# Performance work log

Hardware: AMD Instinct MI355X
Metric: run time of the kernel (lower is better)

Reference implementation:

```python
import jax, jax.numpy as jnp
import numpy as np

N_NODES = 100000
N_EDGES = 1600000
IN_CH, HID_CH, OUT_CH = 128, 128, 64


def _spmm(row, col, val, x, n):
    # COO sparse @ dense: out[r] += val_e * x[col_e]
    gathered = val[:, None] * x[col]  # [E, d]
    return jax.ops.segment_sum(gathered, row, num_segments=n)


def setup_inputs() -> dict:
    key = jax.random.key(0)
    ks = jax.random.split(key, 8)
    x = jax.random.normal(ks[0], (N_NODES, IN_CH), dtype=jnp.float32)
    adj_row = jax.random.randint(ks[1], (N_EDGES,), 0, N_NODES)
    adj_col = jax.random.randint(ks[2], (N_EDGES,), 0, N_NODES)
    adj_val = jax.random.uniform(ks[3], (N_EDGES,), dtype=jnp.float32)
    w1 = jax.random.normal(ks[4], (IN_CH, HID_CH), dtype=jnp.float32) * (1.0 / np.sqrt(IN_CH))
    b1 = jax.random.normal(ks[5], (HID_CH,), dtype=jnp.float32) * 0.01
    w2 = jax.random.normal(ks[6], (HID_CH, OUT_CH), dtype=jnp.float32) * (1.0 / np.sqrt(HID_CH))
    b2 = jax.random.normal(ks[7], (OUT_CH,), dtype=jnp.float32) * 0.01
    return {"x": x, "adj_row": adj_row, "adj_col": adj_col, "adj_val": adj_val,
            "w1": w1, "b1": b1, "w2": w2, "b2": b2}


def reference(x, adj_row, adj_col, adj_val, w1, b1, w2, b2):
    n = x.shape[0]
    # layer 1: spmm -> linear -> relu
    h = _spmm(adj_row, adj_col, adj_val, x, n)
    h = jax.nn.relu(h @ w1 + b1)
    # layer 2: spmm -> linear
    h = _spmm(adj_row, adj_col, adj_val, h, n)
    return h @ w2 + b2
```

## Files before the change

### kernel.cpp

```cpp
#include <hip/hip_runtime.h>


typedef __bf16 v8bf __attribute__((ext_vector_type(8)));
typedef float  v4f  __attribute__((ext_vector_type(4)));
typedef unsigned v2u __attribute__((ext_vector_type(2)));

#define AS1 __attribute__((address_space(1)))
#define AS3 __attribute__((address_space(3)))

#define MAXB 800

__device__ __forceinline__ unsigned short f2bf(float f) {
    unsigned u = __float_as_uint(f);
    unsigned r = u + 0x7fffu + ((u >> 16) & 1u);
    return (unsigned short)(r >> 16);
}

__device__ __forceinline__ unsigned ldsaddr(const void* p) {
    return (unsigned)(unsigned long long)(const AS3 char*)p;
}

__device__ __forceinline__ v2u tr16(unsigned a) {
    v2u d;
    asm volatile("ds_read_b64_tr_b16 %0, %1" : "=v"(d) : "v"(a));
    return d;
}

__global__ __launch_bounds__(256) void hist_prep(const int* __restrict__ arow,
                                                 int* __restrict__ counts, int E, int B,
                                                 const float* __restrict__ w1,
                                                 const float* __restrict__ w2,
                                                 unsigned short* __restrict__ w1T,
                                                 unsigned short* __restrict__ w2T,
                                                 int* __restrict__ rowptr,
                                                 int2* __restrict__ epkS, int N) {
    const int tid = threadIdx.x;
    int gi = blockIdx.x * 256 + tid;
    if (gi < 16384) {
        int n = gi >> 7, k = gi & 127;
        w1T[gi] = f2bf(w1[k * 128 + n]);
    } else if (gi < 24576) {
        int i2 = gi - 16384;
        int n = i2 >> 7, k = i2 & 127;
        w2T[i2] = f2bf(w2[k * 64 + n]);
    } else if (gi < 24576 + 32) {
        epkS[E + (gi - 24576)] = make_int2(0, 0);
    } else if (gi == 24576 + 32) {
        rowptr[N] = E;
    }
    __shared__ int lh[MAXB];
    for (int i = tid; i < B; i += 256) lh[i] = 0;
    __syncthreads();
    const int base = blockIdx.x * 4096;
#pragma unroll
    for (int j = 0; j < 16; ++j) {
        int i = base + j * 256 + tid;
        if (i < E) atomicAdd(&lh[arow[i] >> 7], 1);
    }
    __syncthreads();
    for (int i = tid; i < B; i += 256) {
        int c = lh[i];
        if (c) atomicAdd(&counts[i], c);
    }
}

__global__ __launch_bounds__(256) void scan_s(const int* __restrict__ counts,
                                              int* __restrict__ boff,
                                              int* __restrict__ gcursor, int B, int E) {
    __shared__ int lds[256];
    const int t = threadIdx.x;
    const int b0 = t * 4;
    int v[4];
    int s = 0;
#pragma unroll
    for (int j = 0; j < 4; ++j) {
        v[j] = (b0 + j < B) ? counts[b0 + j] : 0;
        s += v[j];
    }
    lds[t] = s;
    __syncthreads();
    for (int off = 1; off < 256; off <<= 1) {
        int tmp = 0;
        if (t >= off) tmp = lds[t - off];
        __syncthreads();
        if (t >= off) lds[t] += tmp;
        __syncthreads();
    }
    int run = (t > 0) ? lds[t - 1] : 0;
#pragma unroll
    for (int j = 0; j < 4; ++j) {
        if (b0 + j < B) {
            boff[b0 + j] = run;
            gcursor[b0 + j] = run;
        }
        run += v[j];
    }
    if (t == 255) boff[B] = E;
}

__global__ __launch_bounds__(256) void partition_k(const int* __restrict__ arow,
                                                   const int* __restrict__ acol,
                                                   const float* __restrict__ aval,
                                                   int* __restrict__ gcursor,
                                                   int2* __restrict__ epk, int E, int B) {
    __shared__ int2 ldata[4096];
    __shared__ int ldest[4096];
    __shared__ int lhist[MAXB];
    __shared__ int lscan[MAXB];
    __shared__ int ldelta[MAXB];
    __shared__ int lcur[MAXB];
    __shared__ int stmp[256];
    const int tid = threadIdx.x;
    const int base = blockIdx.x * 4096;
    const int cnt = min(4096, E - base);

    for (int i = tid; i < MAXB; i += 256) {
        lhist[i] = 0;
        lcur[i] = 0;
    }
    __syncthreads();

    int rr[16];
#pragma unroll
    for (int j = 0; j < 16; ++j) {
        int i = base + j * 256 + tid;
        rr[j] = (i < E) ? arow[i] : -1;
        if (rr[j] >= 0) atomicAdd(&lhist[rr[j] >> 7], 1);
    }
    __syncthreads();

    const int b0 = tid * 4;
    int v[4];
    int s = 0;
#pragma unroll
    for (int j = 0; j < 4; ++j) {
        v[j] = (b0 + j < MAXB) ? lhist[b0 + j] : 0;
        s += v[j];
    }
    stmp[tid] = s;
    __syncthreads();
    for (int off = 1; off < 256; off <<= 1) {
        int tmp = 0;
        if (tid >= off) tmp = stmp[tid - off];
        __syncthreads();
        if (tid >= off) stmp[tid] += tmp;
        __syncthreads();
    }
    int run = (tid > 0) ? stmp[tid - 1] : 0;
#pragma unroll
    for (int j = 0; j < 4; ++j) {
        if (b0 + j < MAXB) lscan[b0 + j] = run;
        run += v[j];
    }
    __syncthreads();

    for (int b = tid; b < B; b += 256) {
        int c = lhist[b];
        if (c) ldelta[b] = atomicAdd(&gcursor[b], c) - lscan[b];
    }
    __syncthreads();

#pragma unroll
    for (int j = 0; j < 16; ++j) {
        int i = base + j * 256 + tid;
        if (i < E) {
            int r = rr[j];
            int b = r >> 7;
            int lp = atomicAdd(&lcur[b], 1);
            int slot = lscan[b] + lp;
            int pk = acol[i] | ((r & 127) << 17);
            ldata[slot] = make_int2(pk, __float_as_int(aval[i]));
            ldest[slot] = ldelta[b] + slot;
        }
    }
    __syncthreads();

    for (int s2 = tid; s2 < cnt; s2 += 256) epk[ldest[s2]] = ldata[s2];
}

template <int NC, bool AF32>
__device__ __forceinline__ void gemm_body(const void* __restrict__ A,
                                          const unsigned short* __restrict__ wT,
                                          unsigned short* __restrict__ y, int M,
                                          int bid, char* smem) {
    constexpr int KP = 136;
    constexpr int NT = NC / 16;
    unsigned short* wl = (unsigned short*)smem;
    const int tid = threadIdx.x;
    for (int idx = tid; idx < NC * 16; idx += 256) {
        int n = idx >> 4, kc = idx & 15;
        *(uint4*)&wl[n * KP + kc * 8] = *(const uint4*)&wT[n * 128 + kc * 8];
    }
    __syncthreads();

    const int wave = tid >> 6;
    const int lane = tid & 63;
    const int m = lane & 15;
    const int q = lane >> 4;
    const int rowbase = bid * 64 + wave * 16;
    const int rowc = min(rowbase + m, M - 1);

    v4f acc[NT] = {};
    union LU { uint4 qv; v8bf b; };

#pragma unroll
    for (int ks = 0; ks < 4; ++ks) {
        const int k0 = ks * 32 + q * 8;
        v8bf a;
        if (AF32) {
            const float* Ap = (const float*)A + (size_t)rowc * 128 + k0;
            float4 f0 = *(const float4*)Ap;
            float4 f1 = *(const float4*)(Ap + 4);
            union { unsigned short s[8]; v8bf b; } cv;
            cv.s[0] = f2bf(f0.x); cv.s[1] = f2bf(f0.y);
            cv.s[2] = f2bf(f0.z); cv.s[3] = f2bf(f0.w);
            cv.s[4] = f2bf(f1.x); cv.s[5] = f2bf(f1.y);
            cv.s[6] = f2bf(f1.z); cv.s[7] = f2bf(f1.w);
            a = cv.b;
        } else {
            LU lu;
            lu.qv = *(const uint4*)((const unsigned short*)A + (size_t)rowc * 128 + k0);
            a = lu.b;
        }
#pragma unroll
        for (int nt = 0; nt < NT; ++nt) {
            v8bf b = *(const v8bf*)&wl[(nt * 16 + m) * KP + k0];
            acc[nt] = __builtin_amdgcn_mfma_f32_16x16x32_bf16(a, b, acc[nt], 0, 0, 0);
        }
    }
#pragma unroll
    for (int nt = 0; nt < NT; ++nt) {
#pragma unroll
        for (int r = 0; r < 4; ++r) {
            int orow = rowbase + q * 4 + r;
            if (orow < M) y[(size_t)orow * NC + nt * 16 + m] = f2bf(acc[nt][r]);
        }
    }
}

__global__ __launch_bounds__(256) void sort_gemm1(const int* __restrict__ boff,
                                                  const int2* __restrict__ epk,
                                                  int2* __restrict__ epkS,
                                                  int* __restrict__ rowptr, int N, int B,
                                                  const float* __restrict__ x,
                                                  const unsigned short* __restrict__ w1T,
                                                  unsigned short* __restrict__ y1b) {
    __shared__ __align__(16) char smem[34816];
    const int tid = threadIdx.x;
    if (blockIdx.x >= B) {
        gemm_body<128, true>(x, w1T, y1b, N, blockIdx.x - B, smem);
        return;
    }
    int2* sorted = (int2*)smem;
    int*  sc     = (int*)(smem + 32768);
    int*  lcur   = (int*)(smem + 32768 + 512);
    const int b = blockIdx.x;
    const int s = boff[b], e = boff[b + 1];
    const int cnt = min(e - s, 4096);
    if (tid < 128) sc[tid] = 0;
    __syncthreads();
    for (int i = s + tid; i < e; i += 256) {
        int rl = (epk[i].x >> 17) & 127;
        atomicAdd(&sc[rl], 1);
    }
    __syncthreads();
    int hv = (tid < 128) ? sc[tid] : 0;
    for (int off = 1; off < 128; off <<= 1) {
        int add = 0;
        if (tid < 128 && tid >= off) add = sc[tid - off];
        __syncthreads();
        if (tid < 128 && tid >= off) sc[tid] += add;
        __syncthreads();
    }
    if (tid < 128) {
        int ex = sc[tid] - hv;
        lcur[tid] = ex;
        int r = b * 128 + tid;
        if (r < N) rowptr[r] = s + ex;
    }
    __syncthreads();
    for (int i = s + tid; i < e; i += 256) {
        int2 p = epk[i];
        int rl = (p.x >> 17) & 127;
        int slot = atomicAdd(&lcur[rl], 1);
        if (slot < 4096) sorted[slot] = p;
    }
    __syncthreads();
    for (int i = tid; i < cnt; i += 256) epkS[s + i] = sorted[i];
}

__global__ __launch_bounds__(256) void spmm_gemm2(const int* __restrict__ rowptr,
                                                  const int2* __restrict__ ep,
                                                  const unsigned short* __restrict__ y1b,
                                                  const float* __restrict__ b1,
                                                  const unsigned short* __restrict__ w2T,
                                                  unsigned short* __restrict__ y2b, int N) {
    constexpr int KP = 136;
    __shared__ __align__(1024) char smem[40960];
    const int tid = threadIdx.x;
    const int wave = tid >> 6, lane = tid & 63;
    char* NTc = smem + wave * 10240;
    char* AT0 = NTc + 8192;
    char* AT1 = NTc + 9216;
    const int rowbase = blockIdx.x * 64;
    const int r0 = rowbase + wave * 16;
    const int si = __builtin_amdgcn_readfirstlane(rowptr[min(r0, N)]);
    const int ei = __builtin_amdgcn_readfirstlane(rowptr[min(r0 + 16, N)]);
    const int m = lane & 15, q = lane >> 4;

    float b1v[8];
#pragma unroll
    for (int h = 0; h < 8; ++h) b1v[h] = b1[h * 16 + m];

    const unsigned trB = ldsaddr(NTc) + (unsigned)(q * 256 + m * 8);

    v4f acc[8] = {};

    for (int cb = si; cb < ei; cb += 32) {
        const int2 pe = ep[cb + (lane & 31)];
        const int colg = __shfl(pe.x & 0x1FFFF, lane >> 1);
        const char* gp = (const char*)y1b + ((size_t)(unsigned)colg << 8) + ((lane & 1) << 4);
#pragma unroll
        for (int t = 0; t < 8; ++t)
            __builtin_amdgcn_global_load_lds((const AS1 unsigned*)(gp + t * 32),
                                             (AS3 unsigned*)(NTc + t * 1024),
                                             16, 0, 0);
        const uint4 z4 = make_uint4(0u, 0u, 0u, 0u);
        *(uint4*)(AT0 + lane * 16) = z4;
        *(uint4*)(AT1 + lane * 16) = z4;
        if (lane < 32 && cb + lane < ei) {
            const float v = __int_as_float(pe.y);
            const unsigned short vh = f2bf(v);
            const float vhf = __uint_as_float((unsigned)vh << 16);
            const unsigned short vl = f2bf(v - vhf);
            const int rl4 = (pe.x >> 17) & 15;
            *(unsigned short*)(AT0 + rl4 * 64 + lane * 2) = vh;
            *(unsigned short*)(AT1 + rl4 * 64 + lane * 2) = vl;
        }
        asm volatile("s_waitcnt vmcnt(0)" ::: "memory");
        __builtin_amdgcn_sched_barrier(0);
        v2u tr0[8], tr1[8];
#pragma unroll
        for (int h = 0; h < 8; ++h) {
            tr0[h] = tr16(trB + h * 1024);
            tr1[h] = tr16(trB + h * 1024 + 128);
        }
        const v8bf avh = *(const v8bf*)(AT0 + m * 64 + q * 16);
        const v8bf avl = *(const v8bf*)(AT1 + m * 64 + q * 16);
        asm volatile("s_waitcnt lgkmcnt(0)" ::: "memory");
        __builtin_amdgcn_sched_barrier(0);
#pragma unroll
        for (int h = 0; h < 8; ++h) {
            union { unsigned u[4]; v8bf b; } bu;
            bu.u[0] = tr0[h][0]; bu.u[1] = tr0[h][1];
            bu.u[2] = tr1[h][0]; bu.u[3] = tr1[h][1];
            acc[h] = __builtin_amdgcn_mfma_f32_16x16x32_bf16(avh, bu.b, acc[h], 0, 0, 0);
            acc[h] = __builtin_amdgcn_mfma_f32_16x16x32_bf16(avl, bu.b, acc[h], 0, 0, 0);
        }
    }
    __syncthreads();
    unsigned short* h1 = (unsigned short*)smem;
#pragma unroll
    for (int h = 0; h < 8; ++h) {
#pragma unroll
        for (int r = 0; r < 4; ++r) {
            const float f = fmaxf(acc[h][r] + b1v[h], 0.f);
            h1[(wave * 16 + q * 4 + r) * KP + h * 16 + m] = f2bf(f);
        }
    }
    __syncthreads();

    v4f acc2[4] = {};
#pragma unroll
    for (int ks = 0; ks < 4; ++ks) {
        const int k0 = ks * 32 + q * 8;
        v8bf av = *(const v8bf*)&h1[(wave * 16 + m) * KP + k0];
#pragma unroll
        for (int nt = 0; nt < 4; ++nt) {
            v8bf b = *(const v8bf*)&w2T[(nt * 16 + m) * 128 + k0];
            acc2[nt] = __builtin_amdgcn_mfma_f32_16x16x32_bf16(av, b, acc2[nt], 0, 0, 0);
        }
    }
#pragma unroll
    for (int nt = 0; nt < 4; ++nt) {
#pragma unroll
        for (int r = 0; r < 4; ++r) {
            int orow = rowbase + wave * 16 + q * 4 + r;
            if (orow < N) y2b[(size_t)orow * 64 + nt * 16 + m] = f2bf(acc2[nt][r]);
        }
    }
}

__global__ __launch_bounds__(256) void spmm64(const int* __restrict__ rowptr,
                                              const int2* __restrict__ ep,
                                              const unsigned short* __restrict__ yb,
                                              const float* __restrict__ bias,
                                              float* __restrict__ outp, int N) {
    const int row = (blockIdx.x * 256 + threadIdx.x) >> 6;
    const int lane = threadIdx.x & 63;
    if (row >= N) return;
    const int eslot = lane >> 3;
    const int cb = lane & 7;
    const unsigned* y32 = (const unsigned*)yb;
    const int s = __builtin_amdgcn_readfirstlane(rowptr[row]);
    const int e = __builtin_amdgcn_readfirstlane(rowptr[row + 1]);
    float a[8] = {0.f, 0.f, 0.f, 0.f, 0.f, 0.f, 0.f, 0.f};
    int2 cur[2];
#pragma unroll
    for (int k = 0; k < 2; ++k) cur[k] = ep[s + 8 * k + eslot];
    for (int j = s; j < e; j += 16) {
        int2 nxt[2];
#pragma unroll
        for (int k = 0; k < 2; ++k) nxt[k] = ep[j + 16 + 8 * k + eslot];
        uint4 g[2];
        float v[2];
#pragma unroll
        for (int k = 0; k < 2; ++k) {
            v[k] = (j + 8 * k + eslot < e) ? __int_as_float(cur[k].y) : 0.f;
            if (j + 8 * k < e)
                g[k] = *(const uint4*)(y32 + (((unsigned)(cur[k].x & 0x1FFFF)) << 5) + (cb << 2));
            else
                g[k] = make_uint4(0u, 0u, 0u, 0u);
        }
#pragma unroll
        for (int k = 0; k < 2; ++k) {
            a[0] += v[k] * __uint_as_float(g[k].x << 16);
            a[1] += v[k] * __uint_as_float(g[k].x & 0xffff0000u);
            a[2] += v[k] * __uint_as_float(g[k].y << 16);
            a[3] += v[k] * __uint_as_float(g[k].y & 0xffff0000u);
            a[4] += v[k] * __uint_as_float(g[k].z << 16);
            a[5] += v[k] * __uint_as_float(g[k].z & 0xffff0000u);
            a[6] += v[k] * __uint_as_float(g[k].w << 16);
            a[7] += v[k] * __uint_as_float(g[k].w & 0xffff0000u);
        }
#pragma unroll
        for (int k = 0; k < 2; ++k) cur[k] = nxt[k];
    }
#pragma unroll
    for (int t = 0; t < 8; ++t) a[t] += __shfl_xor(a[t], 8);
#pragma unroll
    for (int t = 0; t < 8; ++t) a[t] += __shfl_xor(a[t], 16);
#pragma unroll
    for (int t = 0; t < 8; ++t) a[t] += __shfl_xor(a[t], 32);
    if (lane < 8) {
        const float4 c0 = *(const float4*)&bias[8 * cb];
        const float4 c1 = *(const float4*)&bias[8 * cb + 4];
        float4 o0 = make_float4(a[0] + c0.x, a[1] + c0.y, a[2] + c0.z, a[3] + c0.w);
        float4 o1 = make_float4(a[4] + c1.x, a[5] + c1.y, a[6] + c1.z, a[7] + c1.w);
        float* op = outp + (size_t)row * 64 + 8 * cb;
        *(float4*)op = o0;
        *(float4*)(op + 4) = o1;
    }
}

extern "C" void kernel_launch(void* const* d_in, const int* in_sizes, int n_in,
                              void* d_out, int out_size, void* d_ws, size_t ws_size,
                              hipStream_t stream) {
    const float* x    = (const float*)d_in[0];
    const int*   arow = (const int*)d_in[1];
    const int*   acol = (const int*)d_in[2];
    const float* aval = (const float*)d_in[3];
    const float* w1   = (const float*)d_in[4];
    const float* b1   = (const float*)d_in[5];
    const float* w2   = (const float*)d_in[6];
    const float* b2   = (const float*)d_in[7];
    float*       out  = (float*)d_out;

    const int N = in_sizes[0] / 128;
    const int E = in_sizes[1];
    const int B = (N + 127) >> 7;

    char* p = (char*)d_ws;
    auto alloc = [&](size_t bytes) {
        char* r = p;
        p += (bytes + 255) & ~(size_t)255;
        return r;
    };
    int*            counts  = (int*)alloc((size_t)MAXB * 4);
    int*            boff    = (int*)alloc((size_t)(MAXB + 1) * 4);
    int*            gcursor = (int*)alloc((size_t)MAXB * 4);
    int*            rowptr  = (int*)alloc((size_t)(N + 1) * 4);
    int2*           epkS    = (int2*)alloc((size_t)(E + 32) * 8);
    unsigned short* w1T     = (unsigned short*)alloc(128 * 128 * 2);
    unsigned short* w2T     = (unsigned short*)alloc(64 * 128 * 2);
    unsigned short* y1b     = (unsigned short*)alloc((size_t)N * 128 * 2);
    int2*           epk     = (int2*)alloc((size_t)E * 8);
    unsigned short* y2b     = (unsigned short*)alloc((size_t)N * 64 * 2);

    const int gemm_blocks = (N + 63) / 64;
    const int pb = (E + 4095) / 4096;

    hipMemsetAsync(counts, 0, (size_t)MAXB * 4, stream);
    hist_prep<<<pb, 256, 0, stream>>>(arow, counts, E, B, w1, w2, w1T, w2T,
                                      rowptr, epkS, N);
    scan_s<<<1, 256, 0, stream>>>(counts, boff, gcursor, B, E);
    partition_k<<<pb, 256, 0, stream>>>(arow, acol, aval, gcursor, epk, E, B);
    sort_gemm1<<<B + gemm_blocks, 256, 0, stream>>>(boff, epk, epkS, rowptr, N, B,
                                                    x, w1T, y1b);
    spmm_gemm2<<<gemm_blocks, 256, 0, stream>>>(rowptr, epkS, y1b, b1, w2T, y2b, N);
    const int spmm_blocks = (N + 3) / 4;
    spmm64<<<spmm_blocks, 256, 0, stream>>>(rowptr, epkS, y2b, b2, out, N);
}
```

Measured before the change: 280.9 us.

## Double-buffer SpMM gather DMA and switch second SpMM to MFMA path

```diff
diff --git a/kernel.cpp b/kernel.cpp
--- a/kernel.cpp
+++ b/kernel.cpp
@@ -289,59 +289,70 @@
     for (int i = tid; i < cnt; i += 256) epkS[s + i] = sorted[i];
 }
 
-__global__ __launch_bounds__(256) void spmm_gemm2(const int* __restrict__ rowptr,
-                                                  const int2* __restrict__ ep,
-                                                  const unsigned short* __restrict__ y1b,
-                                                  const float* __restrict__ b1,
-                                                  const unsigned short* __restrict__ w2T,
-                                                  unsigned short* __restrict__ y2b, int N) {
-    constexpr int KP = 136;
-    __shared__ __align__(1024) char smem[40960];
-    const int tid = threadIdx.x;
-    const int wave = tid >> 6, lane = tid & 63;
-    char* NTc = smem + wave * 10240;
-    char* AT0 = NTc + 8192;
-    char* AT1 = NTc + 9216;
-    const int rowbase = blockIdx.x * 64;
-    const int r0 = rowbase + wave * 16;
-    const int si = __builtin_amdgcn_readfirstlane(rowptr[min(r0, N)]);
-    const int ei = __builtin_amdgcn_readfirstlane(rowptr[min(r0 + 16, N)]);
+template <int NT>
+__device__ __forceinline__ void issue_dma(const unsigned short* __restrict__ yb,
+                                          int colg, int lane, char* NB) {
+    const char* gp = (const char*)yb + ((size_t)(unsigned)colg << (NT == 8 ? 8 : 7)) +
+                     ((lane & 1) << 4);
+#pragma unroll
+    for (int t = 0; t < NT; ++t)
+        __builtin_amdgcn_global_load_lds((const AS1 unsigned*)(gp + t * 32),
+                                         (AS3 unsigned*)(NB + t * 1024), 16, 0, 0);
+}
+
+template <int NT>
+__device__ __forceinline__ void spmm_mfma_pipe(int si, int ei, int E,
+                                               const int2* __restrict__ ep,
+                                               const unsigned short* __restrict__ yb,
+                                               char* NB0, char* NB1, char* AT0, char* AT1,
+                                               int lane, v4f* acc) {
     const int m = lane & 15, q = lane >> 4;
-
-    float b1v[8];
-#pragma unroll
-    for (int h = 0; h < 8; ++h) b1v[h] = b1[h * 16 + m];
-
-    const unsigned trB = ldsaddr(NTc) + (unsigned)(q * 256 + m * 8);
-
-    v4f acc[8] = {};
-
-    for (int cb = si; cb < ei; cb += 32) {
-        const int2 pe = ep[cb + (lane & 31)];
-        const int colg = __shfl(pe.x & 0x1FFFF, lane >> 1);
-        const char* gp = (const char*)y1b + ((size_t)(unsigned)colg << 8) + ((lane & 1) << 4);
-#pragma unroll
-        for (int t = 0; t < 8; ++t)
-            __builtin_amdgcn_global_load_lds((const AS1 unsigned*)(gp + t * 32),
-                                             (AS3 unsigned*)(NTc + t * 1024),
-                                             16, 0, 0);
+    const int l31 = lane & 31;
+    const unsigned trBo = (unsigned)(q * 256 + m * 8);
+    const int nch = (ei - si + 31) >> 5;
+    if (nch <= 0) return;
+    int2 peA = ep[min(si + l31, E + 31)];
+    {
+        int colg0 = __shfl(peA.x & 0x1FFFF, lane >> 1);
+        issue_dma<NT>(yb, colg0, lane, NB0);
+    }
+    int2 peB = ep[min(si + 32 + l31, E + 31)];
+#pragma unroll 1
+    for (int c = 0; c < nch; ++c) {
+        char* curN = (c & 1) ? NB1 : NB0;
+        char* nxtN = (c & 1) ? NB0 : NB1;
+        const int cb = si + c * 32;
+        const bool more = (c + 1 < nch);
+        int2 peC = ep[min(cb + 64 + l31, E + 31)];
+        __builtin_amdgcn_sched_barrier(0);
+        if (more) {
+            int colgN = __shfl(peB.x & 0x1FFFF, lane >> 1);
+            issue_dma<NT>(yb, colgN, lane, nxtN);
+        }
+        __builtin_amdgcn_sched_barrier(0);
         const uint4 z4 = make_uint4(0u, 0u, 0u, 0u);
         *(uint4*)(AT0 + lane * 16) = z4;
         *(uint4*)(AT1 + lane * 16) = z4;
-        if (lane < 32 && cb + lane < ei) {
-            const float v = __int_as_float(pe.y);
+        if (lane < 32 && cb + l31 < ei) {
+            const float v = __int_as_float(peA.y);
             const unsigned short vh = f2bf(v);
             const float vhf = __uint_as_float((unsigned)vh << 16);
             const unsigned short vl = f2bf(v - vhf);
-            const int rl4 = (pe.x >> 17) & 15;
-            *(unsigned short*)(AT0 + rl4 * 64 + lane * 2) = vh;
-            *(unsigned short*)(AT1 + rl4 * 64 + lane * 2) = vl;
-        }
-        asm volatile("s_waitcnt vmcnt(0)" ::: "memory");
+            const int rl4 = (peA.x >> 17) & 15;
+            *(unsigned short*)(AT0 + rl4 * 64 + l31 * 2) = vh;
+            *(unsigned short*)(AT1 + rl4 * 64 + l31 * 2) = vl;
+        }
+        if (more) {
+            if constexpr (NT == 8) asm volatile("s_waitcnt vmcnt(9)" ::: "memory");
+            else                   asm volatile("s_waitcnt vmcnt(5)" ::: "memory");
+        } else {
+            asm volatile("s_waitcnt vmcnt(0)" ::: "memory");
+        }
         __builtin_amdgcn_sched_barrier(0);
-        v2u tr0[8], tr1[8];
-#pragma unroll
-        for (int h = 0; h < 8; ++h) {
+        const unsigned trB = ldsaddr(curN) + trBo;
+        v2u tr0[NT], tr1[NT];
+#pragma unroll
+        for (int h = 0; h < NT; ++h) {
             tr0[h] = tr16(trB + h * 1024);
             tr1[h] = tr16(trB + h * 1024 + 128);
         }
@@ -350,21 +361,46 @@
         asm volatile("s_waitcnt lgkmcnt(0)" ::: "memory");
         __builtin_amdgcn_sched_barrier(0);
 #pragma unroll
-        for (int h = 0; h < 8; ++h) {
+        for (int h = 0; h < NT; ++h) {
             union { unsigned u[4]; v8bf b; } bu;
             bu.u[0] = tr0[h][0]; bu.u[1] = tr0[h][1];
             bu.u[2] = tr1[h][0]; bu.u[3] = tr1[h][1];
             acc[h] = __builtin_amdgcn_mfma_f32_16x16x32_bf16(avh, bu.b, acc[h], 0, 0, 0);
             acc[h] = __builtin_amdgcn_mfma_f32_16x16x32_bf16(avl, bu.b, acc[h], 0, 0, 0);
         }
-    }
+        peA = peB;
+        peB = peC;
+    }
+}
+
+__global__ __launch_bounds__(128) void spmm_gemm2(const int* __restrict__ rowptr,
+                                                  const int2* __restrict__ ep,
+                                                  const unsigned short* __restrict__ y1b,
+                                                  const float* __restrict__ b1,
+                                                  const unsigned short* __restrict__ w2T,
+                                                  unsigned short* __restrict__ y2b,
+                                                  int N, int E) {
+    constexpr int KP = 136;
+    __shared__ __align__(1024) char smem[36864];
+    const int tid = threadIdx.x;
+    const int wave = tid >> 6, lane = tid & 63;
+    char* W = smem + wave * 18432;
+    const int rowbase = blockIdx.x * 32;
+    const int r0 = rowbase + wave * 16;
+    const int si = __builtin_amdgcn_readfirstlane(rowptr[min(r0, N)]);
+    const int ei = __builtin_amdgcn_readfirstlane(rowptr[min(r0 + 16, N)]);
+    const int m = lane & 15, q = lane >> 4;
+
+    v4f acc[8] = {};
+    spmm_mfma_pipe<8>(si, ei, E, ep, y1b, W, W + 8192, W + 16384, W + 17408, lane, acc);
     __syncthreads();
     unsigned short* h1 = (unsigned short*)smem;
 #pragma unroll
     for (int h = 0; h < 8; ++h) {
+        const float bv = b1[h * 16 + m];
 #pragma unroll
         for (int r = 0; r < 4; ++r) {
-            const float f = fmaxf(acc[h][r] + b1v[h], 0.f);
+            const float f = fmaxf(acc[h][r] + bv, 0.f);
             h1[(wave * 16 + q * 4 + r) * KP + h * 16 + m] = f2bf(f);
         }
     }
@@ -395,61 +431,27 @@
                                               const int2* __restrict__ ep,
                                               const unsigned short* __restrict__ yb,
                                               const float* __restrict__ bias,
-                                              float* __restrict__ outp, int N) {
-    const int row = (blockIdx.x * 256 + threadIdx.x) >> 6;
-    const int lane = threadIdx.x & 63;
-    if (row >= N) return;
-    const int eslot = lane >> 3;
-    const int cb = lane & 7;
-    const unsigned* y32 = (const unsigned*)yb;
-    const int s = __builtin_amdgcn_readfirstlane(rowptr[row]);
-    const int e = __builtin_amdgcn_readfirstlane(rowptr[row + 1]);
-    float a[8] = {0.f, 0.f, 0.f, 0.f, 0.f, 0.f, 0.f, 0.f};
-    int2 cur[2];
-#pragma unroll
-    for (int k = 0; k < 2; ++k) cur[k] = ep[s + 8 * k + eslot];
-    for (int j = s; j < e; j += 16) {
-        int2 nxt[2];
-#pragma unroll
-        for (int k = 0; k < 2; ++k) nxt[k] = ep[j + 16 + 8 * k + eslot];
-        uint4 g[2];
-        float v[2];
-#pragma unroll
-        for (int k = 0; k < 2; ++k) {
-            v[k] = (j + 8 * k + eslot < e) ? __int_as_float(cur[k].y) : 0.f;
-            if (j + 8 * k < e)
-                g[k] = *(const uint4*)(y32 + (((unsigned)(cur[k].x & 0x1FFFF)) << 5) + (cb << 2));
-            else
-                g[k] = make_uint4(0u, 0u, 0u, 0u);
-        }
-#pragma unroll
-        for (int k = 0; k < 2; ++k) {
-            a[0] += v[k] * __uint_as_float(g[k].x << 16);
-            a[1] += v[k] * __uint_as_float(g[k].x & 0xffff0000u);
-            a[2] += v[k] * __uint_as_float(g[k].y << 16);
-            a[3] += v[k] * __uint_as_float(g[k].y & 0xffff0000u);
-            a[4] += v[k] * __uint_as_float(g[k].z << 16);
-            a[5] += v[k] * __uint_as_float(g[k].z & 0xffff0000u);
-            a[6] += v[k] * __uint_as_float(g[k].w << 16);
-            a[7] += v[k] * __uint_as_float(g[k].w & 0xffff0000u);
-        }
-#pragma unroll
-        for (int k = 0; k < 2; ++k) cur[k] = nxt[k];
-    }
-#pragma unroll
-    for (int t = 0; t < 8; ++t) a[t] += __shfl_xor(a[t], 8);
-#pragma unroll
-    for (int t = 0; t < 8; ++t) a[t] += __shfl_xor(a[t], 16);
-#pragma unroll
-    for (int t = 0; t < 8; ++t) a[t] += __shfl_xor(a[t], 32);
-    if (lane < 8) {
-        const float4 c0 = *(const float4*)&bias[8 * cb];
-        const float4 c1 = *(const float4*)&bias[8 * cb + 4];
-        float4 o0 = make_float4(a[0] + c0.x, a[1] + c0.y, a[2] + c0.z, a[3] + c0.w);
-        float4 o1 = make_float4(a[4] + c1.x, a[5] + c1.y, a[6] + c1.z, a[7] + c1.w);
-        float* op = outp + (size_t)row * 64 + 8 * cb;
-        *(float4*)op = o0;
-        *(float4*)(op + 4) = o1;
+                                              float* __restrict__ outp, int N, int E) {
+    __shared__ __align__(1024) char smem[40960];
+    const int tid = threadIdx.x;
+    const int wave = tid >> 6, lane = tid & 63;
+    char* W = smem + wave * 10240;
+    const int r0 = blockIdx.x * 64 + wave * 16;
+    const int si = __builtin_amdgcn_readfirstlane(rowptr[min(r0, N)]);
+    const int ei = __builtin_amdgcn_readfirstlane(rowptr[min(r0 + 16, N)]);
+    const int m = lane & 15, q = lane >> 4;
+
+    v4f acc[4] = {};
+    spmm_mfma_pipe<4>(si, ei, E, ep, yb, W, W + 4096, W + 8192, W + 9216, lane, acc);
+
+#pragma unroll
+    for (int h = 0; h < 4; ++h) {
+        const float bv = bias[h * 16 + m];
+#pragma unroll
+        for (int r = 0; r < 4; ++r) {
+            const int orow = r0 + q * 4 + r;
+            if (orow < N) outp[(size_t)orow * 64 + h * 16 + m] = acc[h][r] + bv;
+        }
     }
 }
 
@@ -497,7 +499,7 @@
     partition_k<<<pb, 256, 0, stream>>>(arow, acol, aval, gcursor, epk, E, B);
     sort_gemm1<<<B + gemm_blocks, 256, 0, stream>>>(boff, epk, epkS, rowptr, N, B,
                                                     x, w1T, y1b);
-    spmm_gemm2<<<gemm_blocks, 256, 0, stream>>>(rowptr, epkS, y1b, b1, w2T, y2b, N);
-    const int spmm_blocks = (N + 3) / 4;
-    spmm64<<<spmm_blocks, 256, 0, stream>>>(rowptr, epkS, y2b, b2, out, N);
-}
+    const int sg2_blocks = (N + 31) / 32;
+    spmm_gemm2<<<sg2_blocks, 128, 0, stream>>>(rowptr, epkS, y1b, b1, w2T, y2b, N, E);
+    spmm64<<<gemm_blocks, 256, 0, stream>>>(rowptr, epkS, y2b, b2, out, N, E);
+}
```

Measured after the change: 277.3 us. About the same (-1.3%).
